# Kernel tuning notes

Measured on AMD Instinct MI355X. Metric: run time of the kernel, lower is better.

## Reference

```python
import jax, jax.numpy as jnp
import numpy as np

B, S, D = 1, 1024, 2048
H, KVH = 16, 4
HD = D // H            # 128
E, F, TOPK = 8, 2048, 2
CLIP_QKV = 8.0
ROPE_BASE = 500000.0


def _layernorm(x, w):
    # LayerNorm without bias (DBRX norm_1/norm_2)
    mu = jnp.mean(x, axis=-1, keepdims=True)
    var = jnp.mean(jnp.square(x - mu), axis=-1, keepdims=True)
    return (x - mu) * jax.lax.rsqrt(var + 1e-5) * w


def _rope(x, pos):
    # neox-style rotary; x: [B,S,h,HD], pos: [B,S]
    half = HD // 2
    inv_freq = 1.0 / (ROPE_BASE ** (jnp.arange(0, half, dtype=jnp.float32) / half))
    freqs = pos.astype(jnp.float32)[:, :, None] * inv_freq  # [B,S,half]
    cos = jnp.cos(freqs)[:, :, None, :]
    sin = jnp.sin(freqs)[:, :, None, :]
    x1, x2 = x[..., :half], x[..., half:]
    return jnp.concatenate([x1 * cos - x2 * sin, x2 * cos + x1 * sin], axis=-1)


def setup_inputs() -> dict:
    key = jax.random.key(0)
    ks = jax.random.split(key, 8)
    std = 0.02
    return {
        "hidden_states": jax.random.normal(ks[0], (B, S, D), dtype=jnp.float32),
        "attention_mask": jnp.ones((B, S), dtype=jnp.int32),
        "position_ids": jnp.arange(S, dtype=jnp.int32)[None, :].repeat(B, axis=0),
        "norm1_w": jnp.ones((D,), dtype=jnp.float32),
        "norm2_w": jnp.ones((D,), dtype=jnp.float32),
        "wqkv": jax.random.normal(ks[1], (D, D + 2 * KVH * HD), dtype=jnp.float32) * std,
        "out_proj_w": jax.random.normal(ks[2], (D, D), dtype=jnp.float32) * std,
        "router_w": jax.random.normal(ks[3], (D, E), dtype=jnp.float32) * std,
        "w1": jax.random.normal(ks[4], (E, F, D), dtype=jnp.float32) * std,
        "v1": jax.random.normal(ks[5], (E, F, D), dtype=jnp.float32) * std,
        "w2": jax.random.normal(ks[6], (E, F, D), dtype=jnp.float32) * std,
    }


def reference(hidden_states, attention_mask, position_ids, norm1_w, norm2_w,
              wqkv, out_proj_w, router_w, w1, v1, w2):
    x = hidden_states
    # ---- norm_1 + attention ----
    h = _layernorm(x, norm1_w)
    qkv = jnp.clip(h @ wqkv, -CLIP_QKV, CLIP_QKV)
    q = qkv[..., :D].reshape(B, S, H, HD)
    k = qkv[..., D:D + KVH * HD].reshape(B, S, KVH, HD)
    v = qkv[..., D + KVH * HD:].reshape(B, S, KVH, HD)
    q = _rope(q, position_ids)
    k = _rope(k, position_ids)
    # GQA: repeat kv heads
    k = jnp.repeat(k, H // KVH, axis=2)
    v = jnp.repeat(v, H // KVH, axis=2)
    scores = jnp.einsum("bqhd,bkhd->bhqk", q, k) / jnp.sqrt(jnp.float32(HD))
    causal = jnp.tril(jnp.ones((S, S), dtype=bool))
    mask = causal[None, None, :, :] & (attention_mask.astype(bool))[:, None, None, :]
    scores = jnp.where(mask, scores, jnp.finfo(scores.dtype).min)
    probs = jax.nn.softmax(scores, axis=-1)
    attn = jnp.einsum("bhqk,bkhd->bqhd", probs, v).reshape(B, S, D)
    attn_out = attn @ out_proj_w
    resid = x + attn_out
    # ---- norm_2 + MoE FFN ----
    h2 = _layernorm(resid, norm2_w)
    logits = h2 @ router_w
    weights = jax.nn.softmax(logits.astype(jnp.float32), axis=-1)
    top_w, top_e = jax.lax.top_k(weights, TOPK)
    top_w = top_w / jnp.sum(top_w, axis=-1, keepdims=True)  # L1 normalize
    top_w = top_w.astype(x.dtype)
    moe = jnp.zeros_like(h2)
    for e in range(E):  # dense per-expert GLU, masked by router weights (as in source)
        x1 = jax.nn.silu(jnp.einsum("bsd,fd->bsf", h2, w1[e]))
        x2 = jnp.einsum("bsd,fd->bsf", h2, v1[e])
        y = jnp.einsum("bsf,fd->bsd", x1 * x2, w2[e])
        gate = jnp.sum((top_e == e).astype(top_w.dtype) * top_w, axis=-1)
        moe = moe + gate[:, :, None] * y
    return resid + moe
```

## Files before the change

### kernel.cpp

```cpp
#include <hip/hip_runtime.h>
#include <math.h>

#define S 1024
#define DM 2048
#define NH 16
#define NKV 4
#define HD 128
#define NE 8
#define FF 2048
#define QKVN 3072

typedef float f32x4 __attribute__((ext_vector_type(4)));
typedef short bf16x8 __attribute__((ext_vector_type(8)));
typedef unsigned short u16;

__device__ __forceinline__ u16 f2bf(float x) {
    union { float f; unsigned u; } v; v.f = x;
    unsigned r = v.u + 0x7FFFu + ((v.u >> 16) & 1u);
    return (u16)(r >> 16);
}

__device__ __forceinline__ void gl_lds16(const u16* g, u16* l) {
    __builtin_amdgcn_global_load_lds(
        (const __attribute__((address_space(1))) void*)g,
        (__attribute__((address_space(3))) void*)l, 16, 0, 0);
}

enum { EPI_CLIP = 0, EPI_RESID = 1, EPI_SCORES = 2, EPI_BF16 = 3, EPI_F32 = 4,
       EPI_SILUMUL = 5, EPI_SCATTER = 6 };

template<int EPI, bool KLIM, bool GATHER>
__global__ __launch_bounds__(256) void gemm_kernel(
    const u16* __restrict__ Abase, long lda, long strideAz,
    const u16* __restrict__ Bbase, long ldb, long strideBz, int zdivB,
    void* __restrict__ Cbase, long ldc, long strideCz,
    int M, int K,
    const int* __restrict__ a_idx,
    const int* __restrict__ out_idx,
    const float* __restrict__ gatesb,
    const int* __restrict__ cntp,
    const float* __restrict__ aux0, long strideAux,
    float* __restrict__ aux1,
    const int* __restrict__ amask)
{
    const int z = blockIdx.z;
    int Mz = M;
    if (cntp) Mz = cntp[z];
    const int bm = blockIdx.y, bn = blockIdx.x;
    if (bm * 64 >= Mz) return;

    const int tid = threadIdx.x;
    const int lane = tid & 63, wave = tid >> 6;
    const int ln = lane & 15, quad = lane >> 4;
    const int wm = wave >> 1, wn = wave & 1;

    float* Cz = (float*)Cbase + (size_t)z * strideCz;

    if (EPI == EPI_SCORES && bn * 128 >= bm * 64 + 64) {
        const float4 mv = make_float4(-3.0e38f, -3.0e38f, -3.0e38f, -3.0e38f);
        for (int t = tid; t < 64 * 32; t += 256) {
            int row = t >> 5, c4 = (t & 31) * 4;
            *(float4*)&Cz[(size_t)(bm * 64 + row) * ldc + bn * 128 + c4] = mv;
        }
        return;
    }

    __shared__ u16 lA[64 * 32];
    __shared__ u16 lB[128 * 32];

    const u16* A = Abase + (size_t)z * strideAz;
    const u16* B = Bbase + (size_t)(z / zdivB) * strideBz;

    const int am = bm * 64 + wave * 16 + (lane >> 2);
    long arow;
    if (GATHER) arow = (am < Mz) ? (long)a_idx[(size_t)z * S + am] : 0;
    else        arow = (am < Mz) ? (long)am : 0;
    const u16* aptr  = A + arow * lda + (lane & 3) * 8;
    const int bn0 = bn * 128 + wave * 32 + (lane >> 2);
    const u16* bptr0 = B + (size_t)bn0 * ldb + (lane & 3) * 8;
    const u16* bptr1 = bptr0 + (size_t)16 * ldb;
    u16* lAw  = lA + wave * 512;
    u16* lBw0 = lB + wave * 1024;
    u16* lBw1 = lBw0 + 512;

    f32x4 acc[2][4];
#pragma unroll
    for (int i = 0; i < 2; i++)
#pragma unroll
        for (int j = 0; j < 4; j++)
            acc[i][j] = (f32x4){0.f, 0.f, 0.f, 0.f};

    const int kcap = bm * 64 + 64;
    const int kmax = KLIM ? ((K < kcap) ? K : kcap) : K;

    for (int k0 = 0; k0 < kmax; k0 += 32) {
        __syncthreads();
        gl_lds16(aptr + k0, lAw);
        gl_lds16(bptr0 + k0, lBw0);
        gl_lds16(bptr1 + k0, lBw1);
        __syncthreads();
        bf16x8 af[2], bfr[4];
#pragma unroll
        for (int i = 0; i < 2; i++)
            af[i] = *(const bf16x8*)&lA[(wm * 32 + i * 16 + ln) * 32 + quad * 8];
#pragma unroll
        for (int j = 0; j < 4; j++)
            bfr[j] = *(const bf16x8*)&lB[(wn * 64 + j * 16 + ln) * 32 + quad * 8];
#pragma unroll
        for (int i = 0; i < 2; i++)
#pragma unroll
            for (int j = 0; j < 4; j++)
                acc[i][j] = __builtin_amdgcn_mfma_f32_16x16x32_bf16(af[i], bfr[j], acc[i][j], 0, 0, 0);
    }

    const int baserow = bm * 64 + wm * 32;
    const int basecol = bn * 128 + wn * 64;
#pragma unroll
    for (int i = 0; i < 2; i++) {
#pragma unroll
        for (int j = 0; j < 4; j++) {
#pragma unroll
            for (int r = 0; r < 4; r++) {
                int gm = baserow + i * 16 + quad * 4 + r;
                int gn = basecol + j * 16 + ln;
                if (gm >= Mz) continue;
                float v = acc[i][j][r];
                if constexpr (EPI == EPI_CLIP) {
                    Cz[(size_t)gm * ldc + gn] = fminf(fmaxf(v, -8.f), 8.f);
                } else if constexpr (EPI == EPI_SCORES) {
                    float sv = v * 0.08838834764831845f;
                    if (gn > gm || amask[gn] == 0) sv = -3.0e38f;
                    Cz[(size_t)gm * ldc + gn] = sv;
                } else if constexpr (EPI == EPI_RESID) {
                    float r2 = v + aux0[(size_t)gm * ldc + gn];
                    Cz[(size_t)gm * ldc + gn] = r2;
                    aux1[(size_t)gm * ldc + gn] = r2;
                } else if constexpr (EPI == EPI_F32) {
                    Cz[(size_t)gm * ldc + gn] = v;
                } else if constexpr (EPI == EPI_BF16) {
                    u16* C = (u16*)Cbase + (size_t)z * strideCz;
                    C[(size_t)gm * ldc + gn] = f2bf(v);
                } else if constexpr (EPI == EPI_SILUMUL) {
                    float tv = aux0[(size_t)z * strideAux + (size_t)gm * ldc + gn];
                    float sl = tv / (1.f + expf(-tv));
                    u16* C = (u16*)Cbase + (size_t)z * strideCz;
                    C[(size_t)gm * ldc + gn] = f2bf(sl * v);
                } else {
                    int tok = out_idx[(size_t)z * S + gm];
                    float g = gatesb[(size_t)z * S + gm];
                    atomicAdd((float*)Cbase + (size_t)tok * ldc + gn, g * v);
                }
            }
        }
    }
}

__global__ __launch_bounds__(256) void cvt_kernel(
    const float* __restrict__ s, u16* __restrict__ d, long n)
{
    long i = ((long)blockIdx.x * 256 + threadIdx.x) * 8;
    if (i >= n) return;
    float4 a = *(const float4*)(s + i);
    float4 b = *(const float4*)(s + i + 4);
    u16 o[8] = { f2bf(a.x), f2bf(a.y), f2bf(a.z), f2bf(a.w),
                 f2bf(b.x), f2bf(b.y), f2bf(b.z), f2bf(b.w) };
    *(uint4*)(d + i) = *(uint4*)o;
}

__global__ __launch_bounds__(256) void transpose_kernel(
    const float* __restrict__ src, long ldsrc, long srcZ,
    u16* __restrict__ dst, long lddst, long dstZ)
{
    __shared__ u16 t[32][33];
    const float* s = src + (size_t)blockIdx.z * srcZ;
    u16* d = dst + (size_t)blockIdx.z * dstZ;
    int c0 = blockIdx.x * 32, r0 = blockIdx.y * 32;
    int tx = threadIdx.x & 31, ty = threadIdx.x >> 5;
#pragma unroll
    for (int i = 0; i < 32; i += 8)
        t[ty + i][tx] = f2bf(s[(size_t)(r0 + ty + i) * ldsrc + c0 + tx]);
    __syncthreads();
#pragma unroll
    for (int i = 0; i < 32; i += 8)
        d[(size_t)(c0 + ty + i) * lddst + r0 + tx] = t[tx][ty + i];
}

__global__ __launch_bounds__(256) void ln_kernel(
    const float* __restrict__ x, const float* __restrict__ w,
    u16* __restrict__ obf, float* __restrict__ of32)
{
    const int t = blockIdx.x;
    const float* xr = x + (size_t)t * DM;
    __shared__ float red[256];
    float vals[8];
    float s = 0.f, s2 = 0.f;
    for (int i = 0; i < 8; i++) {
        float v = xr[threadIdx.x + i * 256];
        vals[i] = v; s += v; s2 += v * v;
    }
    red[threadIdx.x] = s; __syncthreads();
    for (int st = 128; st > 0; st >>= 1) {
        if (threadIdx.x < st) red[threadIdx.x] += red[threadIdx.x + st];
        __syncthreads();
    }
    float mean = red[0] / DM; __syncthreads();
    red[threadIdx.x] = s2; __syncthreads();
    for (int st = 128; st > 0; st >>= 1) {
        if (threadIdx.x < st) red[threadIdx.x] += red[threadIdx.x + st];
        __syncthreads();
    }
    float var = red[0] / DM - mean * mean;
    float inv = 1.0f / sqrtf(var + 1e-5f);
    for (int i = 0; i < 8; i++) {
        int d = threadIdx.x + i * 256;
        float v = (vals[i] - mean) * inv * w[d];
        obf[(size_t)t * DM + d] = f2bf(v);
        if (of32) of32[(size_t)t * DM + d] = v;
    }
}

__global__ __launch_bounds__(256) void rope_kernel(
    const float* __restrict__ qkv, const int* __restrict__ pos_ids,
    u16* __restrict__ qb, u16* __restrict__ kb)
{
    int id = blockIdx.x * 256 + threadIdx.x;
    if (id >= S * (NH + NKV) * 64) return;
    int i = id & 63;
    int hh = (id >> 6) % (NH + NKV);
    int t = id / ((NH + NKV) * 64);
    float pos = (float)pos_ids[t];
    float invf = powf(500000.0f, -(float)i / 64.0f);
    float f = pos * invf;
    float c = cosf(f), sn = sinf(f);
    const float* base;
    u16* out;
    if (hh < NH) {
        base = qkv + (size_t)t * QKVN + hh * HD;
        out = qb + ((size_t)t * NH + hh) * HD;
    } else {
        int hk = hh - NH;
        base = qkv + (size_t)t * QKVN + DM + hk * HD;
        out = kb + ((size_t)t * NKV + hk) * HD;
    }
    float x1 = base[i], x2 = base[i + 64];
    out[i]      = f2bf(x1 * c - x2 * sn);
    out[i + 64] = f2bf(x2 * c + x1 * sn);
}

__global__ __launch_bounds__(256) void softmax_kernel(
    const float* __restrict__ scores, u16* __restrict__ probs)
{
    const size_t row = blockIdx.x;
    const float* sr = scores + row * S;
    u16* pr = probs + row * S;
    __shared__ float red[256];
    float v[4];
    float m = -3.4e38f;
    for (int i = 0; i < 4; i++) {
        v[i] = sr[threadIdx.x + i * 256];
        m = fmaxf(m, v[i]);
    }
    red[threadIdx.x] = m; __syncthreads();
    for (int st = 128; st > 0; st >>= 1) {
        if (threadIdx.x < st) red[threadIdx.x] = fmaxf(red[threadIdx.x], red[threadIdx.x + st]);
        __syncthreads();
    }
    m = red[0]; __syncthreads();
    float ssum = 0.f; float e[4];
    for (int i = 0; i < 4; i++) { e[i] = expf(v[i] - m); ssum += e[i]; }
    red[threadIdx.x] = ssum; __syncthreads();
    for (int st = 128; st > 0; st >>= 1) {
        if (threadIdx.x < st) red[threadIdx.x] += red[threadIdx.x + st];
        __syncthreads();
    }
    float invl = 1.0f / red[0];
    for (int i = 0; i < 4; i++)
        pr[threadIdx.x + i * 256] = f2bf(e[i] * invl);
}

__global__ void zero_cnt_kernel(int* cnt) {
    if (threadIdx.x < NE) cnt[threadIdx.x] = 0;
}

__global__ __launch_bounds__(64) void router_kernel(
    const float* __restrict__ h2f, const float* __restrict__ rw,
    int* __restrict__ cnt, int* __restrict__ list, float* __restrict__ gates)
{
    const int t = blockIdx.x;
    const int l = threadIdx.x;
    const int e = l >> 3, p = l & 7;
    const float* hr = h2f + (size_t)t * DM;
    float s = 0.f;
    for (int d = p; d < DM; d += 8) s += hr[d] * rw[d * NE + e];
    s += __shfl_xor(s, 1);
    s += __shfl_xor(s, 2);
    s += __shfl_xor(s, 4);
    __shared__ float lg[NE];
    if (p == 0) lg[e] = s;
    __syncthreads();
    if (l == 0) {
        int e0 = 0; float m0 = lg[0];
        for (int q = 1; q < NE; q++) if (lg[q] > m0) { m0 = lg[q]; e0 = q; }
        int e1 = -1; float m1 = -3.4e38f;
        for (int q = 0; q < NE; q++) if (q != e0 && lg[q] > m1) { m1 = lg[q]; e1 = q; }
        float g0 = 1.0f / (1.0f + expf(m1 - m0));
        float g1 = 1.0f - g0;
        int p0 = atomicAdd(&cnt[e0], 1); list[e0 * S + p0] = t; gates[e0 * S + p0] = g0;
        int p1 = atomicAdd(&cnt[e1], 1); list[e1 * S + p1] = t; gates[e1 * S + p1] = g1;
    }
}

extern "C" void kernel_launch(void* const* d_in, const int* in_sizes, int n_in,
                              void* d_out, int out_size, void* d_ws, size_t ws_size,
                              hipStream_t stream)
{
    (void)in_sizes; (void)n_in; (void)out_size; (void)ws_size;
    const float* x     = (const float*)d_in[0];
    const int*   amask = (const int*)d_in[1];
    const int*   pos   = (const int*)d_in[2];
    const float* n1w   = (const float*)d_in[3];
    const float* n2w   = (const float*)d_in[4];
    const float* wqkv  = (const float*)d_in[5];
    const float* wout  = (const float*)d_in[6];
    const float* rw    = (const float*)d_in[7];
    const float* w1    = (const float*)d_in[8];
    const float* v1    = (const float*)d_in[9];
    const float* w2    = (const float*)d_in[10];
    float* out = (float*)d_out;

    char* p = (char*)d_ws;
    auto alloc = [&](size_t bytes) {
        char* r = p;
        p += (bytes + 255) & ~(size_t)255;
        return r;
    };
    float* resid  = (float*)alloc((size_t)S * DM * 4);
    float* h2f    = (float*)alloc((size_t)S * DM * 4);
    u16*   h2b    = (u16*)alloc((size_t)S * DM * 2);
    u16*   h1b    = (u16*)alloc((size_t)S * DM * 2);
    u16*   qb     = (u16*)alloc((size_t)S * NH * HD * 2);
    u16*   kb     = (u16*)alloc((size_t)S * NKV * HD * 2);
    u16*   vT     = (u16*)alloc((size_t)NKV * HD * S * 2);
    u16*   attnb  = (u16*)alloc((size_t)S * DM * 2);
    int*   cnt    = (int*)alloc(NE * 4);
    int*   list   = (int*)alloc((size_t)NE * S * 4);
    float* gates  = (float*)alloc((size_t)NE * S * 4);
    float* qkv    = (float*)alloc((size_t)S * QKVN * 4);
    u16*   wqkvT  = (u16*)alloc((size_t)QKVN * DM * 2);
    u16*   woutT  = (u16*)alloc((size_t)DM * DM * 2);
    u16*   wb     = (u16*)alloc((size_t)NE * FF * DM * 2);
    char*  arena  = alloc((size_t)NH * S * S * 4 + (size_t)NH * S * S * 2);
    float* scores = (float*)arena;
    u16*   probs  = (u16*)(arena + (size_t)NH * S * S * 4);
    float* t1 = (float*)arena;
    u16*   xx = (u16*)(arena + (size_t)NH * S * S * 4);

    transpose_kernel<<<dim3(QKVN / 32, DM / 32, 1), 256, 0, stream>>>(
        wqkv, QKVN, 0, wqkvT, DM, 0);
    transpose_kernel<<<dim3(DM / 32, DM / 32, 1), 256, 0, stream>>>(
        wout, DM, 0, woutT, DM, 0);

    ln_kernel<<<S, 256, 0, stream>>>(x, n1w, h1b, nullptr);
    gemm_kernel<EPI_CLIP, false, false><<<dim3(QKVN / 128, S / 64, 1), 256, 0, stream>>>(
        h1b, DM, 0, wqkvT, DM, 0, 1, qkv, QKVN, 0, S, DM,
        nullptr, nullptr, nullptr, nullptr, nullptr, 0, nullptr, nullptr);
    rope_kernel<<<(S * (NH + NKV) * 64) / 256, 256, 0, stream>>>(qkv, pos, qb, kb);
    transpose_kernel<<<dim3((NKV * HD) / 32, S / 32, 1), 256, 0, stream>>>(
        qkv + DM + NKV * HD, QKVN, 0, vT, S, 0);
    gemm_kernel<EPI_SCORES, false, false><<<dim3(S / 128, S / 64, NH), 256, 0, stream>>>(
        qb, NH * HD, HD, kb, NKV * HD, HD, NH / NKV, scores, S, (long)S * S, S, HD,
        nullptr, nullptr, nullptr, nullptr, nullptr, 0, nullptr, amask);
    softmax_kernel<<<NH * S, 256, 0, stream>>>(scores, probs);
    gemm_kernel<EPI_BF16, true, false><<<dim3(HD / 128, S / 64, NH), 256, 0, stream>>>(
        probs, S, (long)S * S, vT, S, (long)HD * S, NH / NKV, attnb, DM, HD, S, S,
        nullptr, nullptr, nullptr, nullptr, nullptr, 0, nullptr, nullptr);
    gemm_kernel<EPI_RESID, false, false><<<dim3(DM / 128, S / 64, 1), 256, 0, stream>>>(
        attnb, DM, 0, woutT, DM, 0, 1, resid, DM, 0, S, DM,
        nullptr, nullptr, nullptr, nullptr, x, 0, out, nullptr);
    ln_kernel<<<S, 256, 0, stream>>>(resid, n2w, h2b, h2f);
    zero_cnt_kernel<<<1, 64, 0, stream>>>(cnt);
    router_kernel<<<S, 64, 0, stream>>>(h2f, rw, cnt, list, gates);
    cvt_kernel<<<(int)(((long)NE * FF * DM / 8 + 255) / 256), 256, 0, stream>>>(
        w1, wb, (long)NE * FF * DM);
    gemm_kernel<EPI_F32, false, true><<<dim3(FF / 128, S / 64, NE), 256, 0, stream>>>(
        h2b, DM, 0, wb, DM, (long)FF * DM, 1, t1, FF, (long)S * FF, S, DM,
        list, nullptr, nullptr, cnt, nullptr, 0, nullptr, nullptr);
    cvt_kernel<<<(int)(((long)NE * FF * DM / 8 + 255) / 256), 256, 0, stream>>>(
        v1, wb, (long)NE * FF * DM);
    gemm_kernel<EPI_SILUMUL, false, true><<<dim3(FF / 128, S / 64, NE), 256, 0, stream>>>(
        h2b, DM, 0, wb, DM, (long)FF * DM, 1, xx, FF, (long)S * FF, S, DM,
        list, nullptr, nullptr, cnt, t1, (long)S * FF, nullptr, nullptr);
    transpose_kernel<<<dim3(DM / 32, FF / 32, NE), 256, 0, stream>>>(
        w2, DM, (long)FF * DM, wb, FF, (long)DM * FF);
    gemm_kernel<EPI_SCATTER, false, false><<<dim3(DM / 128, S / 64, NE), 256, 0, stream>>>(
        xx, FF, (long)S * FF, wb, FF, (long)DM * FF, 1, out, DM, 0, S, FF,
        nullptr, list, gates, cnt, nullptr, 0, nullptr, nullptr);
}
```

Measured before the change: 929.1 us.

## Double-buffer GEMM LDS tiles, skip masked score tiles, streamline softmax and router

The GEMM kernel now double-buffers its A and B LDS tiles. It prefetches the next K slice while running MFMAs on the current one, which cuts the barriers per iteration from two to one. Fully masked causal score tiles are no longer filled with -inf. Instead, the softmax reads and writes only the causal width each row needs, using wave-shuffle reductions. The router processes four tokens per block with vectorized loads and shuffle reductions, and the expert-count zeroing is folded into the second layernorm launch. Together these target memory-stall time in the GEMMs, wasted score writes and reads, and small-kernel launch overhead, at the cost of doubled LDS usage, which could reduce occupancy.

```diff
diff --git a/kernel.cpp b/kernel.cpp
--- a/kernel.cpp
+++ b/kernel.cpp
@@ -48,6 +48,7 @@
     if (cntp) Mz = cntp[z];
     const int bm = blockIdx.y, bn = blockIdx.x;
     if (bm * 64 >= Mz) return;
+    if (EPI == EPI_SCORES && bn * 128 >= bm * 64 + 64) return;
 
     const int tid = threadIdx.x;
     const int lane = tid & 63, wave = tid >> 6;
@@ -56,17 +57,8 @@
 
     float* Cz = (float*)Cbase + (size_t)z * strideCz;
 
-    if (EPI == EPI_SCORES && bn * 128 >= bm * 64 + 64) {
-        const float4 mv = make_float4(-3.0e38f, -3.0e38f, -3.0e38f, -3.0e38f);
-        for (int t = tid; t < 64 * 32; t += 256) {
-            int row = t >> 5, c4 = (t & 31) * 4;
-            *(float4*)&Cz[(size_t)(bm * 64 + row) * ldc + bn * 128 + c4] = mv;
-        }
-        return;
-    }
-
-    __shared__ u16 lA[64 * 32];
-    __shared__ u16 lB[128 * 32];
+    __shared__ u16 lA[2 * 64 * 32];
+    __shared__ u16 lB[2 * 128 * 32];
 
     const u16* A = Abase + (size_t)z * strideAz;
     const u16* B = Bbase + (size_t)(z / zdivB) * strideBz;
@@ -93,24 +85,35 @@
     const int kcap = bm * 64 + 64;
     const int kmax = KLIM ? ((K < kcap) ? K : kcap) : K;
 
+    gl_lds16(aptr, lAw);
+    gl_lds16(bptr0, lBw0);
+    gl_lds16(bptr1, lBw1);
+
+    int buf = 0;
     for (int k0 = 0; k0 < kmax; k0 += 32) {
         __syncthreads();
-        gl_lds16(aptr + k0, lAw);
-        gl_lds16(bptr0 + k0, lBw0);
-        gl_lds16(bptr1 + k0, lBw1);
-        __syncthreads();
+        const int kn = k0 + 32;
+        if (kn < kmax) {
+            const int nb = buf ^ 1;
+            gl_lds16(aptr + kn, lAw + nb * 2048);
+            gl_lds16(bptr0 + kn, lBw0 + nb * 4096);
+            gl_lds16(bptr1 + kn, lBw1 + nb * 4096);
+        }
+        const u16* cA = lA + buf * 2048;
+        const u16* cB = lB + buf * 4096;
         bf16x8 af[2], bfr[4];
 #pragma unroll
         for (int i = 0; i < 2; i++)
-            af[i] = *(const bf16x8*)&lA[(wm * 32 + i * 16 + ln) * 32 + quad * 8];
+            af[i] = *(const bf16x8*)&cA[(wm * 32 + i * 16 + ln) * 32 + quad * 8];
 #pragma unroll
         for (int j = 0; j < 4; j++)
-            bfr[j] = *(const bf16x8*)&lB[(wn * 64 + j * 16 + ln) * 32 + quad * 8];
+            bfr[j] = *(const bf16x8*)&cB[(wn * 64 + j * 16 + ln) * 32 + quad * 8];
 #pragma unroll
         for (int i = 0; i < 2; i++)
 #pragma unroll
             for (int j = 0; j < 4; j++)
                 acc[i][j] = __builtin_amdgcn_mfma_f32_16x16x32_bf16(af[i], bfr[j], acc[i][j], 0, 0, 0);
+        buf ^= 1;
     }
 
     const int baserow = bm * 64 + wm * 32;
@@ -187,9 +190,10 @@
 
 __global__ __launch_bounds__(256) void ln_kernel(
     const float* __restrict__ x, const float* __restrict__ w,
-    u16* __restrict__ obf, float* __restrict__ of32)
+    u16* __restrict__ obf, float* __restrict__ of32, int* __restrict__ cnt0)
 {
     const int t = blockIdx.x;
+    if (cnt0 && t == 0 && threadIdx.x < NE) cnt0[threadIdx.x] = 0;
     const float* xr = x + (size_t)t * DM;
     __shared__ float red[256];
     float vals[8];
@@ -250,59 +254,73 @@
 __global__ __launch_bounds__(256) void softmax_kernel(
     const float* __restrict__ scores, u16* __restrict__ probs)
 {
-    const size_t row = blockIdx.x;
-    const float* sr = scores + row * S;
-    u16* pr = probs + row * S;
-    __shared__ float red[256];
-    float v[4];
-    float m = -3.4e38f;
-    for (int i = 0; i < 4; i++) {
-        v[i] = sr[threadIdx.x + i * 256];
-        m = fmaxf(m, v[i]);
-    }
-    red[threadIdx.x] = m; __syncthreads();
-    for (int st = 128; st > 0; st >>= 1) {
-        if (threadIdx.x < st) red[threadIdx.x] = fmaxf(red[threadIdx.x], red[threadIdx.x + st]);
-        __syncthreads();
-    }
-    m = red[0]; __syncthreads();
-    float ssum = 0.f; float e[4];
-    for (int i = 0; i < 4; i++) { e[i] = expf(v[i] - m); ssum += e[i]; }
-    red[threadIdx.x] = ssum; __syncthreads();
-    for (int st = 128; st > 0; st >>= 1) {
-        if (threadIdx.x < st) red[threadIdx.x] += red[threadIdx.x + st];
-        __syncthreads();
-    }
-    float invl = 1.0f / red[0];
-    for (int i = 0; i < 4; i++)
-        pr[threadIdx.x + i * 256] = f2bf(e[i] * invl);
-}
-
-__global__ void zero_cnt_kernel(int* cnt) {
-    if (threadIdx.x < NE) cnt[threadIdx.x] = 0;
-}
-
-__global__ __launch_bounds__(64) void router_kernel(
+    const int row = blockIdx.x & (S - 1);
+    const size_t base = (size_t)blockIdx.x * S;
+    const int NW = (((row >> 6) * 64 + 64 + 127) >> 7) << 7;
+    const float* sr = scores + base;
+    u16* pr = probs + base;
+    const int t4 = threadIdx.x * 4;
+    const int lane = threadIdx.x & 63, wave = threadIdx.x >> 6;
+    float4 v;
+    if (t4 < NW) v = *(const float4*)(sr + t4);
+    else v = make_float4(-3.4e38f, -3.4e38f, -3.4e38f, -3.4e38f);
+    __shared__ float red[8];
+    float m = fmaxf(fmaxf(v.x, v.y), fmaxf(v.z, v.w));
+#pragma unroll
+    for (int off = 32; off >= 1; off >>= 1) m = fmaxf(m, __shfl_xor(m, off));
+    if (lane == 0) red[wave] = m;
+    __syncthreads();
+    m = fmaxf(fmaxf(red[0], red[1]), fmaxf(red[2], red[3]));
+    float e0 = expf(v.x - m), e1 = expf(v.y - m), e2 = expf(v.z - m), e3 = expf(v.w - m);
+    float s = e0 + e1 + e2 + e3;
+#pragma unroll
+    for (int off = 32; off >= 1; off >>= 1) s += __shfl_xor(s, off);
+    __syncthreads();
+    if (lane == 0) red[4 + wave] = s;
+    __syncthreads();
+    float invl = 1.0f / (red[4] + red[5] + red[6] + red[7]);
+    if (t4 < NW) {
+        u16 o[4] = { f2bf(e0 * invl), f2bf(e1 * invl), f2bf(e2 * invl), f2bf(e3 * invl) };
+        *(unsigned long long*)(pr + t4) = *(unsigned long long*)o;
+    }
+}
+
+__global__ __launch_bounds__(256) void router_kernel(
     const float* __restrict__ h2f, const float* __restrict__ rw,
     int* __restrict__ cnt, int* __restrict__ list, float* __restrict__ gates)
 {
-    const int t = blockIdx.x;
-    const int l = threadIdx.x;
-    const int e = l >> 3, p = l & 7;
+    const int t = blockIdx.x * 4 + (threadIdx.x >> 6);
+    const int lane = threadIdx.x & 63;
     const float* hr = h2f + (size_t)t * DM;
-    float s = 0.f;
-    for (int d = p; d < DM; d += 8) s += hr[d] * rw[d * NE + e];
-    s += __shfl_xor(s, 1);
-    s += __shfl_xor(s, 2);
-    s += __shfl_xor(s, 4);
-    __shared__ float lg[NE];
-    if (p == 0) lg[e] = s;
-    __syncthreads();
-    if (l == 0) {
-        int e0 = 0; float m0 = lg[0];
-        for (int q = 1; q < NE; q++) if (lg[q] > m0) { m0 = lg[q]; e0 = q; }
+    float acc[NE];
+#pragma unroll
+    for (int e = 0; e < NE; e++) acc[e] = 0.f;
+#pragma unroll
+    for (int i = 0; i < 8; i++) {
+        int d0 = i * 256 + lane * 4;
+        float4 h = *(const float4*)(hr + d0);
+        float hv[4] = { h.x, h.y, h.z, h.w };
+#pragma unroll
+        for (int j = 0; j < 4; j++) {
+            const float4 r0 = *(const float4*)(rw + (size_t)(d0 + j) * NE);
+            const float4 r1 = *(const float4*)(rw + (size_t)(d0 + j) * NE + 4);
+            acc[0] += hv[j] * r0.x; acc[1] += hv[j] * r0.y;
+            acc[2] += hv[j] * r0.z; acc[3] += hv[j] * r0.w;
+            acc[4] += hv[j] * r1.x; acc[5] += hv[j] * r1.y;
+            acc[6] += hv[j] * r1.z; acc[7] += hv[j] * r1.w;
+        }
+    }
+#pragma unroll
+    for (int off = 32; off >= 1; off >>= 1)
+#pragma unroll
+        for (int e = 0; e < NE; e++) acc[e] += __shfl_xor(acc[e], off);
+    if (lane == 0) {
+        int e0 = 0; float m0 = acc[0];
+#pragma unroll
+        for (int q = 1; q < NE; q++) if (acc[q] > m0) { m0 = acc[q]; e0 = q; }
         int e1 = -1; float m1 = -3.4e38f;
-        for (int q = 0; q < NE; q++) if (q != e0 && lg[q] > m1) { m1 = lg[q]; e1 = q; }
+#pragma unroll
+        for (int q = 0; q < NE; q++) if (q != e0 && acc[q] > m1) { m1 = acc[q]; e1 = q; }
         float g0 = 1.0f / (1.0f + expf(m1 - m0));
         float g1 = 1.0f - g0;
         int p0 = atomicAdd(&cnt[e0], 1); list[e0 * S + p0] = t; gates[e0 * S + p0] = g0;
@@ -360,7 +378,7 @@
     transpose_kernel<<<dim3(DM / 32, DM / 32, 1), 256, 0, stream>>>(
         wout, DM, 0, woutT, DM, 0);
 
-    ln_kernel<<<S, 256, 0, stream>>>(x, n1w, h1b, nullptr);
+    ln_kernel<<<S, 256, 0, stream>>>(x, n1w, h1b, nullptr, nullptr);
     gemm_kernel<EPI_CLIP, false, false><<<dim3(QKVN / 128, S / 64, 1), 256, 0, stream>>>(
         h1b, DM, 0, wqkvT, DM, 0, 1, qkv, QKVN, 0, S, DM,
         nullptr, nullptr, nullptr, nullptr, nullptr, 0, nullptr, nullptr);
@@ -377,9 +395,8 @@
     gemm_kernel<EPI_RESID, false, false><<<dim3(DM / 128, S / 64, 1), 256, 0, stream>>>(
         attnb, DM, 0, woutT, DM, 0, 1, resid, DM, 0, S, DM,
         nullptr, nullptr, nullptr, nullptr, x, 0, out, nullptr);
-    ln_kernel<<<S, 256, 0, stream>>>(resid, n2w, h2b, h2f);
-    zero_cnt_kernel<<<1, 64, 0, stream>>>(cnt);
-    router_kernel<<<S, 64, 0, stream>>>(h2f, rw, cnt, list, gates);
+    ln_kernel<<<S, 256, 0, stream>>>(resid, n2w, h2b, h2f, cnt);
+    router_kernel<<<S / 4, 256, 0, stream>>>(h2f, rw, cnt, list, gates);
     cvt_kernel<<<(int)(((long)NE * FF * DM / 8 + 255) / 256), 256, 0, stream>>>(
         w1, wb, (long)NE * FF * DM);
     gemm_kernel<EPI_F32, false, true><<<dim3(FF / 128, S / 64, NE), 256, 0, stream>>>(
```

Result: faster. 871.6 us (-6.2%).
